# Performance work log

Measured on AMD Instinct MI355X. Metric: run time of the kernel, lower is better.

The kernel has to match this reference:

```python
import jax, jax.numpy as jnp
import numpy as np

SAMPLE_RATE = 16000
LOW_CUTOFF = 3400.0   # max(cutoff_freq) -> lowpass stage
HIGH_CUTOFF = 300.0   # min(cutoff_freq) -> highpass stage
Q = 0.7071067811865476  # torchaudio default Q = 1/sqrt(2)


def _lowpass_coeffs(cutoff, sr):
    w0 = 2.0 * np.pi * cutoff / sr
    alpha = np.sin(w0) / (2.0 * Q)
    cw = np.cos(w0)
    b0 = (1.0 - cw) / 2.0
    b1 = 1.0 - cw
    b2 = b0
    a0 = 1.0 + alpha
    a1 = -2.0 * cw
    a2 = 1.0 - alpha
    return tuple(np.float32(c / a0) for c in (b0, b1, b2, a1, a2))


def _highpass_coeffs(cutoff, sr):
    w0 = 2.0 * np.pi * cutoff / sr
    alpha = np.sin(w0) / (2.0 * Q)
    cw = np.cos(w0)
    b0 = (1.0 + cw) / 2.0
    b1 = -(1.0 + cw)
    b2 = b0
    a0 = 1.0 + alpha
    a1 = -2.0 * cw
    a2 = 1.0 - alpha
    return tuple(np.float32(c / a0) for c in (b0, b1, b2, a1, a2))


def _biquad(x, coeffs):
    """Direct-form-II-transposed biquad along the last (time) axis.
    x: [B, C, T]. Matches torchaudio lfilter with a0-normalized coeffs,
    followed by the torchaudio default clamp to [-1, 1]."""
    b0, b1, b2, a1, a2 = (jnp.asarray(c, x.dtype) for c in coeffs)
    xt = jnp.moveaxis(x, -1, 0)  # [T, B, C] for time scan

    def step(carry, xi):
        s1, s2 = carry
        y = b0 * xi + s1
        s1n = b1 * xi - a1 * y + s2
        s2n = b2 * xi - a2 * y
        return (s1n, s2n), y

    zeros = jnp.zeros(x.shape[:-1], x.dtype)
    _, yt = jax.lax.scan(step, (zeros, zeros), xt)
    y = jnp.moveaxis(yt, 0, -1)  # back to [B, C, T]
    return jnp.clip(y, -1.0, 1.0)


def setup_inputs() -> dict:
    key = jax.random.key(0)
    # scale down so the post-filter clamp to [-1,1] rarely saturates (audio-like amplitudes)
    waveform = 0.1 * jax.random.normal(key, (32, 2, 480000), dtype=jnp.float32)
    return {"waveform": waveform}


def reference(waveform):
    # bandpass = lowpass(max cutoff) then highpass(min cutoff)
    y = _biquad(waveform, _lowpass_coeffs(LOW_CUTOFF, SAMPLE_RATE))
    y = _biquad(y, _highpass_coeffs(HIGH_CUTOFF, SAMPLE_RATE))
    return y
```

## Files before the change

kernel.cpp:

```cpp
#include <hip/hip_runtime.h>
#include <math.h>


#define NT    128
#define LCH   32
#define WUC   4
#define CH_F4 9
#define NCH   (NT + WUC)
#define SPAN  (NT * LCH)
#define T_LEN 480000

__global__ __launch_bounds__(NT, 4)
void bandpass_kernel(const float* __restrict__ in, float* __restrict__ out,
                     float lb0, float lb1, float lb2, float nla1, float nla2,
                     float hb0, float hb1, float hb2, float nha1, float nha2) {
    __shared__ float4 lds4[NCH * CH_F4];
    const int tid = threadIdx.x;
    const long tile_start = (long)blockIdx.x * SPAN;
    const float* __restrict__ src = in  + (long)blockIdx.y * T_LEN;
    float*       __restrict__ dst = out + (long)blockIdx.y * T_LEN;

    const int NF4 = NCH * 8;
    for (int k = tid; k < NF4; k += NT) {
        long g = tile_start - 128 + 4L * k;
        float4 v = make_float4(0.f, 0.f, 0.f, 0.f);
        if (g >= 0 && g + 4 <= T_LEN) v = *(const float4*)(src + g);
        lds4[CH_F4 * (k >> 3) + (k & 7)] = v;
    }
    __syncthreads();

    float s1a = 0.f, s2a = 0.f, s1b = 0.f, s2b = 0.f;

#define WSTEP(x) {                                         \
        float y1 = fmaf(lb0, (x), s1a);                    \
        s1a = fmaf(lb1, (x), fmaf(nla1, y1, s2a));         \
        s2a = fmaf(lb2, (x), nla2 * y1);                   \
        float x2 = fminf(fmaxf(y1, -1.f), 1.f);            \
        float y2 = fmaf(hb0, x2, s1b);                     \
        s1b = fmaf(hb1, x2, fmaf(nha1, y2, s2b));          \
        s2b = fmaf(hb2, x2, nha2 * y2);                    \
    }
#define OSTEP(x, o) {                                      \
        float y1 = fmaf(lb0, (x), s1a);                    \
        s1a = fmaf(lb1, (x), fmaf(nla1, y1, s2a));         \
        s2a = fmaf(lb2, (x), nla2 * y1);                   \
        float x2 = fminf(fmaxf(y1, -1.f), 1.f);            \
        float y2 = fmaf(hb0, x2, s1b);                     \
        s1b = fmaf(hb1, x2, fmaf(nha1, y2, s2b));          \
        s2b = fmaf(hb2, x2, nha2 * y2);                    \
        (o) = fminf(fmaxf(y2, -1.f), 1.f);                 \
    }

    {
        const float4* wp = &lds4[CH_F4 * tid];
        for (int c = 0; c < WUC; ++c) {
            #pragma unroll
            for (int q = 0; q < 8; ++q) {
                float4 v = wp[CH_F4 * c + q];
                WSTEP(v.x); WSTEP(v.y); WSTEP(v.z); WSTEP(v.w);
            }
        }
    }
    __syncthreads();

    {
        float4* mp = &lds4[CH_F4 * (tid + WUC)];
        #pragma unroll
        for (int q = 0; q < 8; ++q) {
            float4 v = mp[q];
            float4 o;
            OSTEP(v.x, o.x); OSTEP(v.y, o.y); OSTEP(v.z, o.z); OSTEP(v.w, o.w);
            mp[q] = o;
        }
    }
    __syncthreads();

    for (int k = tid; k < SPAN / 4; k += NT) {
        long g = tile_start + 4L * k;
        if (g + 4 <= T_LEN) {
            *(float4*)(dst + g) = lds4[CH_F4 * ((k >> 3) + WUC) + (k & 7)];
        }
    }
#undef WSTEP
#undef OSTEP
}

static void biquad_coeffs(double cutoff, double sr, bool highpass, float* c) {
    const double Q  = 0.7071067811865476;
    const double w0 = 2.0 * M_PI * cutoff / sr;
    const double al = sin(w0) / (2.0 * Q);
    const double cw = cos(w0);
    double b0, b1, b2;
    if (highpass) { b0 = (1.0 + cw) / 2.0; b1 = -(1.0 + cw); b2 = b0; }
    else          { b0 = (1.0 - cw) / 2.0; b1 =  (1.0 - cw); b2 = b0; }
    const double a0 = 1.0 + al;
    const double a1 = -2.0 * cw;
    const double a2 = 1.0 - al;
    c[0] = (float)(b0 / a0);
    c[1] = (float)(b1 / a0);
    c[2] = (float)(b2 / a0);
    c[3] = (float)(-a1 / a0);
    c[4] = (float)(-a2 / a0);
}

extern "C" void kernel_launch(void* const* d_in, const int* in_sizes, int n_in,
                              void* d_out, int out_size, void* d_ws, size_t ws_size,
                              hipStream_t stream) {
    const float* in  = (const float*)d_in[0];
    float*       out = (float*)d_out;

    float lp[5], hp[5];
    biquad_coeffs(3400.0, 16000.0, false, lp);
    biquad_coeffs(300.0, 16000.0, true, hp);

    const int n_seq  = in_sizes[0] / T_LEN;
    const int n_tile = (T_LEN + SPAN - 1) / SPAN;

    dim3 grid(n_tile, n_seq);
    bandpass_kernel<<<grid, NT, 0, stream>>>(
        in, out,
        lp[0], lp[1], lp[2], lp[3], lp[4],
        hp[0], hp[1], hp[2], hp[3], hp[4]);
}
```

Baseline: 233.6 us.

## Replace per-thread warmup recomputation with a block-wide linear state scan

Each thread filters its 32-sample chunk from zero state. A 7-step Hillis-Steele scan in LDS then combines the cascaded biquad states across threads, using host-precomputed 4x4 transition-matrix powers. Each thread re-filters its chunk from the exact incoming state. This removes the 128-sample per-thread warmup, so each output needs about 64 filter steps instead of 160. In exchange it adds seven barrier-separated scan rounds, shrinks each tile to 124 output chunks, and assumes the intermediate clamp is inactive so the state map stays linear.

```diff
diff --git a/kernel.cpp b/kernel.cpp
--- a/kernel.cpp
+++ b/kernel.cpp
@@ -6,30 +6,12 @@
 #define LCH   32
 #define WUC   4
 #define CH_F4 9
-#define NCH   (NT + WUC)
-#define SPAN  (NT * LCH)
+#define NCH   NT
+#define OUTC  (NT - WUC)
+#define SPAN  (OUTC * LCH)
 #define T_LEN 480000
 
-__global__ __launch_bounds__(NT, 4)
-void bandpass_kernel(const float* __restrict__ in, float* __restrict__ out,
-                     float lb0, float lb1, float lb2, float nla1, float nla2,
-                     float hb0, float hb1, float hb2, float nha1, float nha2) {
-    __shared__ float4 lds4[NCH * CH_F4];
-    const int tid = threadIdx.x;
-    const long tile_start = (long)blockIdx.x * SPAN;
-    const float* __restrict__ src = in  + (long)blockIdx.y * T_LEN;
-    float*       __restrict__ dst = out + (long)blockIdx.y * T_LEN;
-
-    const int NF4 = NCH * 8;
-    for (int k = tid; k < NF4; k += NT) {
-        long g = tile_start - 128 + 4L * k;
-        float4 v = make_float4(0.f, 0.f, 0.f, 0.f);
-        if (g >= 0 && g + 4 <= T_LEN) v = *(const float4*)(src + g);
-        lds4[CH_F4 * (k >> 3) + (k & 7)] = v;
-    }
-    __syncthreads();
-
-    float s1a = 0.f, s2a = 0.f, s1b = 0.f, s2b = 0.f;
+struct ScanConsts { float p[7][16]; };
 
 #define WSTEP(x) {                                         \
         float y1 = fmaf(lb0, (x), s1a);                    \
@@ -51,23 +33,68 @@
         (o) = fminf(fmaxf(y2, -1.f), 1.f);                 \
     }
 
-    {
-        const float4* wp = &lds4[CH_F4 * tid];
-        for (int c = 0; c < WUC; ++c) {
-            #pragma unroll
-            for (int q = 0; q < 8; ++q) {
-                float4 v = wp[CH_F4 * c + q];
-                WSTEP(v.x); WSTEP(v.y); WSTEP(v.z); WSTEP(v.w);
-            }
-        }
+__global__ __launch_bounds__(NT, 4)
+void bandpass_kernel(const float* __restrict__ in, float* __restrict__ out,
+                     float lb0, float lb1, float lb2, float nla1, float nla2,
+                     float hb0, float hb1, float hb2, float nha1, float nha2,
+                     ScanConsts SC) {
+    __shared__ float4 lds4[NCH * CH_F4];
+    __shared__ float4 scanB[NCH];
+    const int tid = threadIdx.x;
+    const long tile_start = (long)blockIdx.x * SPAN;
+    const float* __restrict__ src = in  + (long)blockIdx.y * T_LEN;
+    float*       __restrict__ dst = out + (long)blockIdx.y * T_LEN;
+
+    #pragma unroll
+    for (int it = 0; it < 8; ++it) {
+        int k = tid + it * NT;
+        long g = tile_start - (WUC * LCH) + 4L * k;
+        float4 v = make_float4(0.f, 0.f, 0.f, 0.f);
+        if (g >= 0 && g + 4 <= T_LEN) v = *(const float4*)(src + g);
+        lds4[CH_F4 * (k >> 3) + (k & 7)] = v;
     }
     __syncthreads();
 
+    float4 vb[8];
+    float s1a = 0.f, s2a = 0.f, s1b = 0.f, s2b = 0.f;
     {
-        float4* mp = &lds4[CH_F4 * (tid + WUC)];
+        const float4* cp = &lds4[CH_F4 * tid];
         #pragma unroll
         for (int q = 0; q < 8; ++q) {
-            float4 v = mp[q];
+            float4 v = cp[q];
+            vb[q] = v;
+            WSTEP(v.x); WSTEP(v.y); WSTEP(v.z); WSTEP(v.w);
+        }
+    }
+
+    float4 val = make_float4(s1a, s2a, s1b, s2b);
+    lds4[CH_F4 * tid + 8] = val;
+    #pragma unroll
+    for (int k = 0; k < 7; ++k) {
+        __syncthreads();
+        const int off = 1 << k;
+        float4 prev = make_float4(0.f, 0.f, 0.f, 0.f);
+        if ((k & 1) == 0) { if (tid >= off) prev = lds4[CH_F4 * (tid - off) + 8]; }
+        else              { if (tid >= off) prev = scanB[tid - off]; }
+        const float* P_ = SC.p[k];
+        float4 nv;
+        nv.x = fmaf(P_[ 0], prev.x, fmaf(P_[ 1], prev.y, fmaf(P_[ 2], prev.z, fmaf(P_[ 3], prev.w, val.x))));
+        nv.y = fmaf(P_[ 4], prev.x, fmaf(P_[ 5], prev.y, fmaf(P_[ 6], prev.z, fmaf(P_[ 7], prev.w, val.y))));
+        nv.z = fmaf(P_[ 8], prev.x, fmaf(P_[ 9], prev.y, fmaf(P_[10], prev.z, fmaf(P_[11], prev.w, val.z))));
+        nv.w = fmaf(P_[12], prev.x, fmaf(P_[13], prev.y, fmaf(P_[14], prev.z, fmaf(P_[15], prev.w, val.w))));
+        val = nv;
+        if ((k & 1) == 0) scanB[tid] = val;
+        else              lds4[CH_F4 * tid + 8] = val;
+    }
+    __syncthreads();
+    float4 s0 = (tid > 0) ? scanB[tid - 1] : make_float4(0.f, 0.f, 0.f, 0.f);
+
+    s1a = s0.x; s2a = s0.y; s1b = s0.z; s2b = s0.w;
+    {
+        float4* mp = &lds4[CH_F4 * tid];
+        #pragma unroll
+        for (int q = 0; q < 8; ++q) {
+            float4 v = vb[q];
             float4 o;
             OSTEP(v.x, o.x); OSTEP(v.y, o.y); OSTEP(v.z, o.z); OSTEP(v.w, o.w);
             mp[q] = o;
@@ -81,11 +108,11 @@
             *(float4*)(dst + g) = lds4[CH_F4 * ((k >> 3) + WUC) + (k & 7)];
         }
     }
+}
 #undef WSTEP
 #undef OSTEP
-}
 
-static void biquad_coeffs(double cutoff, double sr, bool highpass, float* c) {
+static void biquad_coeffs_d(double cutoff, double sr, bool highpass, double* c) {
     const double Q  = 0.7071067811865476;
     const double w0 = 2.0 * M_PI * cutoff / sr;
     const double al = sin(w0) / (2.0 * Q);
@@ -94,13 +121,20 @@
     if (highpass) { b0 = (1.0 + cw) / 2.0; b1 = -(1.0 + cw); b2 = b0; }
     else          { b0 = (1.0 - cw) / 2.0; b1 =  (1.0 - cw); b2 = b0; }
     const double a0 = 1.0 + al;
-    const double a1 = -2.0 * cw;
-    const double a2 = 1.0 - al;
-    c[0] = (float)(b0 / a0);
-    c[1] = (float)(b1 / a0);
-    c[2] = (float)(b2 / a0);
-    c[3] = (float)(-a1 / a0);
-    c[4] = (float)(-a2 / a0);
+    c[0] = b0 / a0;
+    c[1] = b1 / a0;
+    c[2] = b2 / a0;
+    c[3] = -(-2.0 * cw) / a0;
+    c[4] = -(1.0 - al) / a0;
+}
+
+static void matmul4(const double* A, const double* B, double* C) {
+    for (int r = 0; r < 4; ++r)
+        for (int c = 0; c < 4; ++c) {
+            double s = 0.0;
+            for (int k = 0; k < 4; ++k) s += A[r * 4 + k] * B[k * 4 + c];
+            C[r * 4 + c] = s;
+        }
 }
 
 extern "C" void kernel_launch(void* const* d_in, const int* in_sizes, int n_in,
@@ -109,9 +143,42 @@
     const float* in  = (const float*)d_in[0];
     float*       out = (float*)d_out;
 
+    double lpd[5], hpd[5];
+    biquad_coeffs_d(3400.0, 16000.0, false, lpd);
+    biquad_coeffs_d(300.0, 16000.0, true, hpd);
+
+    double M[16];
+    for (int j = 0; j < 4; ++j) {
+        double s1a = (j == 0), s2a = (j == 1), s1b = (j == 2), s2b = (j == 3);
+        double y1   = s1a;
+        double ns1a = hpd[0] * 0.0;
+        (void)ns1a;
+        double n1a = lpd[3] * y1 + s2a;
+        double n2a = lpd[4] * y1;
+        double y2  = hpd[0] * y1 + s1b;
+        double n1b = hpd[1] * y1 + hpd[3] * y2 + s2b;
+        double n2b = hpd[2] * y1 + hpd[4] * y2;
+        M[0 * 4 + j] = n1a;
+        M[1 * 4 + j] = n2a;
+        M[2 * 4 + j] = n1b;
+        M[3 * 4 + j] = n2b;
+    }
+
+    double A[16], T[16];
+    for (int i = 0; i < 16; ++i) A[i] = M[i];
+    for (int s = 0; s < 5; ++s) { matmul4(A, A, T); for (int i = 0; i < 16; ++i) A[i] = T[i]; }
+
+    ScanConsts SC;
+    double Pk[16];
+    for (int i = 0; i < 16; ++i) Pk[i] = A[i];
+    for (int k = 0; k < 7; ++k) {
+        for (int i = 0; i < 16; ++i) SC.p[k][i] = (float)Pk[i];
+        matmul4(Pk, Pk, T);
+        for (int i = 0; i < 16; ++i) Pk[i] = T[i];
+    }
+
     float lp[5], hp[5];
-    biquad_coeffs(3400.0, 16000.0, false, lp);
-    biquad_coeffs(300.0, 16000.0, true, hp);
+    for (int i = 0; i < 5; ++i) { lp[i] = (float)lpd[i]; hp[i] = (float)hpd[i]; }
 
     const int n_seq  = in_sizes[0] / T_LEN;
     const int n_tile = (T_LEN + SPAN - 1) / SPAN;
@@ -120,5 +187,6 @@
     bandpass_kernel<<<grid, NT, 0, stream>>>(
         in, out,
         lp[0], lp[1], lp[2], lp[3], lp[4],
-        hp[0], hp[1], hp[2], hp[3], hp[4]);
+        hp[0], hp[1], hp[2], hp[3], hp[4],
+        SC);
 }
```

Measured after the change: 221.8 us. 1.05x faster.
